# Optimization experiments

Hardware: AMD Instinct MI355X
Metric: run time of the kernel (lower is better)

The kernel has to match this reference:

```python
import jax, jax.numpy as jnp
import numpy as np

N = 100000
E = 1000000
F_NODE = 64
F_EDGE = 32
H = 128
C_NODE = 12
C_EDGE = 4


def _glorot(key, shape):
    fan_in, fan_out = shape[0], shape[1]
    s = (6.0 / (fan_in + fan_out)) ** 0.5
    return jax.random.uniform(key, shape, jnp.float32, -s, s)


def setup_inputs() -> dict:
    key = jax.random.key(0)
    ks = jax.random.split(key, 16)
    x = jax.random.normal(ks[0], (N, F_NODE), jnp.float32)
    edge_index = jax.random.randint(ks[1], (2, E), 0, N, jnp.int32)
    edge_attr = jax.random.normal(ks[2], (E, F_EDGE), jnp.float32)
    return {
        "x": x,
        "edge_index": edge_index,
        "edge_attr": edge_attr,
        "We": _glorot(ks[3], (F_NODE, H)), "be": jnp.zeros((H,), jnp.float32),
        "Wc1": _glorot(ks[4], (H, H)), "bc1": jnp.zeros((H,), jnp.float32),
        "Wc2": _glorot(ks[5], (H, H)), "bc2": jnp.zeros((H,), jnp.float32),
        "Wn1": _glorot(ks[6], (H, H // 2)), "bn1": jnp.zeros((H // 2,), jnp.float32),
        "Wn2": _glorot(ks[7], (H // 2, C_NODE)), "bn2": jnp.zeros((C_NODE,), jnp.float32),
        "Wedge1": _glorot(ks[8], (2 * H + F_EDGE, H)), "bedge1": jnp.zeros((H,), jnp.float32),
        "Wedge2": _glorot(ks[9], (H, C_EDGE)), "bedge2": jnp.zeros((C_EDGE,), jnp.float32),
    }


def _gcn_conv(x, W, b, src, tgt, n):
    # PyG GCNConv: add self-loops, symmetric deg normalization, scatter-add.
    xw = x @ W  # [N, H]
    loop = jnp.arange(n, dtype=src.dtype)
    s = jnp.concatenate([src, loop])
    t = jnp.concatenate([tgt, loop])
    deg = jax.ops.segment_sum(jnp.ones_like(t, jnp.float32), t, num_segments=n)
    dinv = jnp.where(deg > 0, jax.lax.rsqrt(jnp.maximum(deg, 1.0)), 0.0)
    norm = dinv[s] * dinv[t]  # [E+N]
    msg = xw[s] * norm[:, None]
    return jax.ops.segment_sum(msg, t, num_segments=n) + b


def reference(x, edge_index, edge_attr, We, be, Wc1, bc1, Wc2, bc2,
              Wn1, bn1, Wn2, bn2, Wedge1, bedge1, Wedge2, bedge2):
    n = x.shape[0]
    row, col = edge_index[0], edge_index[1]
    h = jax.nn.relu(x @ We + be)          # node_embed Linear+ReLU
    h = jax.nn.relu(h)                     # extra F.relu in forward
    h = jax.nn.relu(_gcn_conv(h, Wc1, bc1, row, col, n))
    h = jax.nn.relu(_gcn_conv(h, Wc2, bc2, row, col, n))
    node_logits = jax.nn.relu(h @ Wn1 + bn1) @ Wn2 + bn2
    e = jnp.concatenate([h[row], h[col], edge_attr], axis=-1)  # [E, 2H+Fe]
    edge_logits = jax.nn.relu(e @ Wedge1 + bedge1) @ Wedge2 + bedge2
    return (node_logits, edge_logits)
```

## Files before the change

### kernel.cpp

```cpp
#include <hip/hip_runtime.h>

#define N_NODES 100000
#define N_EDGES 1000000
#define NB_SCAN 391
#define EDGE_OUT_BASE 1200000

typedef __attribute__((ext_vector_type(8))) short short8;
typedef __attribute__((ext_vector_type(4))) unsigned short us4;
typedef __attribute__((ext_vector_type(4))) float f32x4;

__device__ __forceinline__ float bf2f(unsigned short u) {
    unsigned int x = ((unsigned int)u) << 16;
    return __builtin_bit_cast(float, x);
}
__device__ __forceinline__ float lo_bf(unsigned int u) {
    return __builtin_bit_cast(float, u << 16);
}
__device__ __forceinline__ float hi_bf(unsigned int u) {
    return __builtin_bit_cast(float, u & 0xffff0000u);
}
__device__ __forceinline__ unsigned short f2bf(float f) {
    unsigned int x = __builtin_bit_cast(unsigned int, f);
    return (unsigned short)((x + 0x7fffu + ((x >> 16) & 1u)) >> 16);
}

__global__ __launch_bounds__(256) void k_detect(const unsigned short* __restrict__ xr,
                                                int* __restrict__ flag) {
    __shared__ int s[256];
    int t = threadIdx.x;
    int cnt = 0;
    for (int i = t; i < 8192; i += 256) {
        int e = (xr[i] >> 7) & 0xFF;
        if (e >= 148) cnt++;
    }
    s[t] = cnt;
    __syncthreads();
    for (int off = 128; off > 0; off >>= 1) {
        if (t < off) s[t] += s[t + off];
        __syncthreads();
    }
    if (t == 0) *flag = (s[0] > 100) ? 1 : 0;
}

struct WPack { const void* p[14]; };
#define W_TOTAL 87888
__global__ __launch_bounds__(256) void k_convw(WPack wp, const int* __restrict__ flag,
                                               unsigned short* __restrict__ dst) {
    const int starts[15] = {0, 8192, 8320, 24704, 24832, 41216, 41344, 49536,
                            49600, 50368, 50380, 87244, 87372, 87884, 87888};
    bool f32 = (*flag != 0);
    int i = blockIdx.x * 256 + threadIdx.x;
    if (i >= W_TOTAL) return;
    int s = 0;
#pragma unroll
    for (int k = 1; k < 14; k++) s += (i >= starts[k]) ? 1 : 0;
    int j = i - starts[s];
    dst[i] = f32 ? f2bf(((const float*)wp.p[s])[j]) : ((const unsigned short*)wp.p[s])[j];
}
#define OW_We 0
#define OW_be 8192
#define OW_Wc1 8320
#define OW_bc1 24704
#define OW_Wc2 24832
#define OW_bc2 41216
#define OW_Wn1 41344
#define OW_bn1 49536
#define OW_Wn2 49600
#define OW_bn2 50368
#define OW_We1 50380
#define OW_be1 87244
#define OW_We2 87372
#define OW_be2 87884

__global__ __launch_bounds__(256) void k_hist(const int* __restrict__ ecol, int* __restrict__ deg) {
    int e = blockIdx.x * 256 + threadIdx.x;
    if (e < N_EDGES) atomicAdd(&deg[ecol[e]], 1);
}

__global__ __launch_bounds__(256) void k_scanA(const int* __restrict__ deg, int* __restrict__ bsum) {
    __shared__ int s[256];
    int i = blockIdx.x * 256 + threadIdx.x;
    s[threadIdx.x] = (i < N_NODES) ? deg[i] : 0;
    __syncthreads();
    for (int off = 128; off > 0; off >>= 1) {
        if (threadIdx.x < off) s[threadIdx.x] += s[threadIdx.x + off];
        __syncthreads();
    }
    if (threadIdx.x == 0) bsum[blockIdx.x] = s[0];
}

__global__ __launch_bounds__(512) void k_scanB(int* __restrict__ bsum) {
    __shared__ int s[512];
    int t = threadIdx.x;
    int v = (t < NB_SCAN) ? bsum[t] : 0;
    s[t] = v;
    __syncthreads();
    for (int off = 1; off < 512; off <<= 1) {
        int x = (t >= off) ? s[t - off] : 0;
        __syncthreads();
        s[t] += x;
        __syncthreads();
    }
    if (t < NB_SCAN) bsum[t] = s[t] - v;
}

__global__ __launch_bounds__(256) void k_scanC(const int* __restrict__ deg, const int* __restrict__ bsum,
                                               int* __restrict__ row_off, int* __restrict__ cursor,
                                               float* __restrict__ dinv) {
    __shared__ int s[256];
    int i = blockIdx.x * 256 + threadIdx.x;
    int t = threadIdx.x;
    int v = (i < N_NODES) ? deg[i] : 0;
    s[t] = v;
    __syncthreads();
    for (int off = 1; off < 256; off <<= 1) {
        int x = (t >= off) ? s[t - off] : 0;
        __syncthreads();
        s[t] += x;
        __syncthreads();
    }
    int excl = s[t] - v + bsum[blockIdx.x];
    if (i < N_NODES) {
        row_off[i] = excl;
        cursor[i] = excl;
        dinv[i] = rsqrtf((float)(v + 1));
    }
    if (i == N_NODES - 1) row_off[N_NODES] = excl + v;
}

__global__ __launch_bounds__(256) void k_fill(const int* __restrict__ erow, const int* __restrict__ ecol,
                                              int* __restrict__ cursor, int* __restrict__ csr) {
    int e = blockIdx.x * 256 + threadIdx.x;
    if (e < N_EDGES) {
        int pos = atomicAdd(&cursor[ecol[e]], 1);
        csr[pos] = erow[e];
    }
}

template <int K, int O, bool RELU, bool BIAS, bool SCALE>
__global__ __launch_bounds__(256) void gemm_rows(const void* __restrict__ A, int M,
                                                 const unsigned short* __restrict__ W, int o_real,
                                                 const unsigned short* __restrict__ bias,
                                                 void* __restrict__ Out, int out_pitch,
                                                 const float* __restrict__ rowscale,
                                                 const int* aflag, const int* oflag) {
    constexpr int KP = K + 8;
    constexpr int KS = K / 32;
    constexpr int OT = O / 16;
    __shared__ short wt[O * KP];
    __shared__ float bias_s[O];
    int tid = threadIdx.x;
    for (int idx = tid; idx < K * O; idx += 256) {
        int k = idx / O, o = idx % O;
        short w = 0;
        if (o < o_real) w = (short)W[(size_t)k * o_real + o];
        wt[o * KP + k] = w;
    }
    if (BIAS) {
        for (int o = tid; o < O; o += 256) bias_s[o] = (o < o_real) ? bf2f(bias[o]) : 0.f;
    }
    __syncthreads();

    bool af32 = aflag && (*aflag != 0);
    bool of32 = oflag && (*oflag != 0);

    int wid = tid >> 6, lane = tid & 63;
    int rbase = (blockIdx.x * 4 + wid) * 32;
    if (rbase >= M) return;
    int lq = lane >> 4, lr = lane & 15;

    short8 a[2][KS];
#pragma unroll
    for (int rg = 0; rg < 2; rg++) {
        int row = rbase + rg * 16 + lr;
        if (row >= M) row = M - 1;
        if (af32) {
            const float* ap = (const float*)A + (size_t)row * K + lq * 8;
#pragma unroll
            for (int ks = 0; ks < KS; ks++) {
                f32x4 u0 = *(const f32x4*)(ap + ks * 32);
                f32x4 u1 = *(const f32x4*)(ap + ks * 32 + 4);
                short8 v;
                v[0] = (short)f2bf(u0[0]); v[1] = (short)f2bf(u0[1]);
                v[2] = (short)f2bf(u0[2]); v[3] = (short)f2bf(u0[3]);
                v[4] = (short)f2bf(u1[0]); v[5] = (short)f2bf(u1[1]);
                v[6] = (short)f2bf(u1[2]); v[7] = (short)f2bf(u1[3]);
                a[rg][ks] = v;
            }
        } else {
            const unsigned short* ap = (const unsigned short*)A + (size_t)row * K + lq * 8;
#pragma unroll
            for (int ks = 0; ks < KS; ks++) a[rg][ks] = *(const short8*)(ap + ks * 32);
        }
    }

    f32x4 acc[2][OT];
#pragma unroll
    for (int rg = 0; rg < 2; rg++)
#pragma unroll
        for (int j = 0; j < OT; j++) {
            acc[rg][j][0] = 0.f; acc[rg][j][1] = 0.f; acc[rg][j][2] = 0.f; acc[rg][j][3] = 0.f;
        }

#pragma unroll
    for (int j = 0; j < OT; j++) {
        short8 b[KS];
#pragma unroll
        for (int ks = 0; ks < KS; ks++)
            b[ks] = *(const short8*)(&wt[(lr + 16 * j) * KP + ks * 32 + lq * 8]);
#pragma unroll
        for (int rg = 0; rg < 2; rg++)
#pragma unroll
            for (int ks = 0; ks < KS; ks++)
                acc[rg][j] = __builtin_amdgcn_mfma_f32_16x16x32_bf16(a[rg][ks], b[ks], acc[rg][j], 0, 0, 0);
    }

#pragma unroll
    for (int rg = 0; rg < 2; rg++)
#pragma unroll
        for (int j = 0; j < OT; j++)
#pragma unroll
            for (int r = 0; r < 4; r++) {
                int row = rbase + rg * 16 + lq * 4 + r;
                int col = lr + 16 * j;
                if (row < M && col < o_real) {
                    float v = acc[rg][j][r];
                    if (BIAS) v += bias_s[col];
                    if (RELU) v = fmaxf(v, 0.f);
                    if (SCALE) v *= rowscale[row];
                    size_t oi = (size_t)row * out_pitch + col;
                    if (of32) ((float*)Out)[oi] = v;
                    else ((unsigned short*)Out)[oi] = f2bf(v);
                }
            }
}

__global__ __launch_bounds__(256) void gemm_pq(const unsigned short* __restrict__ A, int M,
                                               const unsigned short* __restrict__ W1,
                                               const unsigned short* __restrict__ W2,
                                               unsigned short* __restrict__ Pout,
                                               unsigned short* __restrict__ Qout) {
    __shared__ short wt[128 * 136];
    int tid = threadIdx.x;
    int wid = tid >> 6, lane = tid & 63;
    int rbase = (blockIdx.x * 4 + wid) * 32;
    int lq = lane >> 4, lr = lane & 15;

    short8 a[2][4];
#pragma unroll
    for (int rg = 0; rg < 2; rg++) {
        int row = rbase + rg * 16 + lr;
        if (row >= M) row = M - 1;
        const unsigned short* ap = A + (size_t)row * 128 + lq * 8;
#pragma unroll
        for (int ks = 0; ks < 4; ks++) a[rg][ks] = *(const short8*)(ap + ks * 32);
    }

    int pc0 = (lr >> 2) * 32 + (lr & 3);

    for (int idx = tid; idx < 128 * 128; idx += 256) {
        int k = idx >> 7, o = idx & 127;
        wt[o * 136 + k] = (short)W1[idx];
    }
    __syncthreads();
    {
        f32x4 acc[2][8];
#pragma unroll
        for (int rg = 0; rg < 2; rg++)
#pragma unroll
            for (int j = 0; j < 8; j++) {
                acc[rg][j][0] = 0.f; acc[rg][j][1] = 0.f; acc[rg][j][2] = 0.f; acc[rg][j][3] = 0.f;
            }
#pragma unroll
        for (int j = 0; j < 8; j++) {
            short8 b[4];
#pragma unroll
            for (int ks = 0; ks < 4; ks++)
                b[ks] = *(const short8*)(&wt[(lr + 16 * j) * 136 + ks * 32 + lq * 8]);
#pragma unroll
            for (int rg = 0; rg < 2; rg++)
#pragma unroll
                for (int ks = 0; ks < 4; ks++)
                    acc[rg][j] = __builtin_amdgcn_mfma_f32_16x16x32_bf16(a[rg][ks], b[ks], acc[rg][j], 0, 0, 0);
        }
#pragma unroll
        for (int rg = 0; rg < 2; rg++)
#pragma unroll
            for (int j = 0; j < 8; j++)
#pragma unroll
                for (int r = 0; r < 4; r++) {
                    int row = rbase + rg * 16 + lq * 4 + r;
                    if (row < M) Pout[(size_t)row * 128 + pc0 + j * 4] = f2bf(acc[rg][j][r]);
                }
    }
    __syncthreads();

    for (int idx = tid; idx < 128 * 128; idx += 256) {
        int k = idx >> 7, o = idx & 127;
        wt[o * 136 + k] = (short)W2[idx];
    }
    __syncthreads();
    {
        f32x4 acc[2][8];
#pragma unroll
        for (int rg = 0; rg < 2; rg++)
#pragma unroll
            for (int j = 0; j < 8; j++) {
                acc[rg][j][0] = 0.f; acc[rg][j][1] = 0.f; acc[rg][j][2] = 0.f; acc[rg][j][3] = 0.f;
            }
#pragma unroll
        for (int j = 0; j < 8; j++) {
            short8 b[4];
#pragma unroll
            for (int ks = 0; ks < 4; ks++)
                b[ks] = *(const short8*)(&wt[(lr + 16 * j) * 136 + ks * 32 + lq * 8]);
#pragma unroll
            for (int rg = 0; rg < 2; rg++)
#pragma unroll
                for (int ks = 0; ks < 4; ks++)
                    acc[rg][j] = __builtin_amdgcn_mfma_f32_16x16x32_bf16(a[rg][ks], b[ks], acc[rg][j], 0, 0, 0);
        }
#pragma unroll
        for (int rg = 0; rg < 2; rg++)
#pragma unroll
            for (int j = 0; j < 8; j++)
#pragma unroll
                for (int r = 0; r < 4; r++) {
                    int row = rbase + rg * 16 + lq * 4 + r;
                    if (row < M) Qout[(size_t)row * 128 + pc0 + j * 4] = f2bf(acc[rg][j][r]);
                }
    }
}

__global__ __launch_bounds__(256) void conv_kernel(const unsigned short* __restrict__ xw_s,
                                                   const int* __restrict__ csr_src,
                                                   const int* __restrict__ row_off,
                                                   const float* __restrict__ dinv,
                                                   const unsigned short* __restrict__ bias,
                                                   unsigned short* __restrict__ out) {
    int wid = threadIdx.x >> 6, lane = threadIdx.x & 63;
    int base = (blockIdx.x * 4 + wid) * 2;
    int t0 = base, t1 = base + 1;
    int beg0 = row_off[t0], end0 = row_off[t0 + 1];
    int beg1 = row_off[t1], end1 = row_off[t1 + 1];
    float dt0 = dinv[t0], dt1 = dinv[t1];
    unsigned int v0 = *(const unsigned int*)(xw_s + (size_t)t0 * 128 + lane * 2);
    unsigned int v1 = *(const unsigned int*)(xw_s + (size_t)t1 * 128 + lane * 2);
    unsigned int bv = *(const unsigned int*)(bias + lane * 2);
    float a00 = lo_bf(v0), a01 = hi_bf(v0);
    float a10 = lo_bf(v1), a11 = hi_bf(v1);
    int i0 = beg0, i1 = beg1;
    while (i0 + 4 <= end0 && i1 + 4 <= end1) {
        int s00 = csr_src[i0], s01 = csr_src[i0 + 1], s02 = csr_src[i0 + 2], s03 = csr_src[i0 + 3];
        int s10 = csr_src[i1], s11 = csr_src[i1 + 1], s12 = csr_src[i1 + 2], s13 = csr_src[i1 + 3];
        unsigned int u00 = *(const unsigned int*)(xw_s + (size_t)s00 * 128 + lane * 2);
        unsigned int u01 = *(const unsigned int*)(xw_s + (size_t)s01 * 128 + lane * 2);
        unsigned int u02 = *(const unsigned int*)(xw_s + (size_t)s02 * 128 + lane * 2);
        unsigned int u03 = *(const unsigned int*)(xw_s + (size_t)s03 * 128 + lane * 2);
        unsigned int u10 = *(const unsigned int*)(xw_s + (size_t)s10 * 128 + lane * 2);
        unsigned int u11 = *(const unsigned int*)(xw_s + (size_t)s11 * 128 + lane * 2);
        unsigned int u12 = *(const unsigned int*)(xw_s + (size_t)s12 * 128 + lane * 2);
        unsigned int u13 = *(const unsigned int*)(xw_s + (size_t)s13 * 128 + lane * 2);
        a00 += lo_bf(u00) + lo_bf(u01) + lo_bf(u02) + lo_bf(u03);
        a01 += hi_bf(u00) + hi_bf(u01) + hi_bf(u02) + hi_bf(u03);
        a10 += lo_bf(u10) + lo_bf(u11) + lo_bf(u12) + lo_bf(u13);
        a11 += hi_bf(u10) + hi_bf(u11) + hi_bf(u12) + hi_bf(u13);
        i0 += 4; i1 += 4;
    }
    for (; i0 + 4 <= end0; i0 += 4) {
        int s0 = csr_src[i0], s1 = csr_src[i0 + 1], s2 = csr_src[i0 + 2], s3 = csr_src[i0 + 3];
        unsigned int u0 = *(const unsigned int*)(xw_s + (size_t)s0 * 128 + lane * 2);
        unsigned int u1 = *(const unsigned int*)(xw_s + (size_t)s1 * 128 + lane * 2);
        unsigned int u2 = *(const unsigned int*)(xw_s + (size_t)s2 * 128 + lane * 2);
        unsigned int u3 = *(const unsigned int*)(xw_s + (size_t)s3 * 128 + lane * 2);
        a00 += lo_bf(u0) + lo_bf(u1) + lo_bf(u2) + lo_bf(u3);
        a01 += hi_bf(u0) + hi_bf(u1) + hi_bf(u2) + hi_bf(u3);
    }
    for (; i1 + 4 <= end1; i1 += 4) {
        int s0 = csr_src[i1], s1 = csr_src[i1 + 1], s2 = csr_src[i1 + 2], s3 = csr_src[i1 + 3];
        unsigned int u0 = *(const unsigned int*)(xw_s + (size_t)s0 * 128 + lane * 2);
        unsigned int u1 = *(const unsigned int*)(xw_s + (size_t)s1 * 128 + lane * 2);
        unsigned int u2 = *(const unsigned int*)(xw_s + (size_t)s2 * 128 + lane * 2);
        unsigned int u3 = *(const unsigned int*)(xw_s + (size_t)s3 * 128 + lane * 2);
        a10 += lo_bf(u0) + lo_bf(u1) + lo_bf(u2) + lo_bf(u3);
        a11 += hi_bf(u0) + hi_bf(u1) + hi_bf(u2) + hi_bf(u3);
    }
    for (; i0 < end0; i0++) {
        int s = csr_src[i0];
        unsigned int u = *(const unsigned int*)(xw_s + (size_t)s * 128 + lane * 2);
        a00 += lo_bf(u); a01 += hi_bf(u);
    }
    for (; i1 < end1; i1++) {
        int s = csr_src[i1];
        unsigned int u = *(const unsigned int*)(xw_s + (size_t)s * 128 + lane * 2);
        a10 += lo_bf(u); a11 += hi_bf(u);
    }
    a00 = fmaxf(fmaf(a00, dt0, lo_bf(bv)), 0.f);
    a01 = fmaxf(fmaf(a01, dt0, hi_bf(bv)), 0.f);
    a10 = fmaxf(fmaf(a10, dt1, lo_bf(bv)), 0.f);
    a11 = fmaxf(fmaf(a11, dt1, hi_bf(bv)), 0.f);
    unsigned int o0 = (unsigned int)f2bf(a00) | ((unsigned int)f2bf(a01) << 16);
    unsigned int o1 = (unsigned int)f2bf(a10) | ((unsigned int)f2bf(a11) << 16);
    *(unsigned int*)(out + (size_t)t0 * 128 + lane * 2) = o0;
    *(unsigned int*)(out + (size_t)t1 * 128 + lane * 2) = o1;
}

__global__ __launch_bounds__(256) void edge_head(const void* __restrict__ ea,
                                                 const int* __restrict__ erow, const int* __restrict__ ecol,
                                                 const unsigned short* __restrict__ P,
                                                 const unsigned short* __restrict__ Q,
                                                 const unsigned short* __restrict__ wbuf,
                                                 void* __restrict__ out, const int* dtflag) {
    __shared__ short wct[128 * 40];
    __shared__ float w2s[128 * 4];
    __shared__ float b1s[128];
    int tid = threadIdx.x;
    const unsigned short* Wc3 = wbuf + OW_We1 + 256 * 128;
    for (int idx = tid; idx < 32 * 128; idx += 256) {
        int k = idx >> 7, o = idx & 127;
        wct[o * 40 + k] = (short)Wc3[idx];
    }
    for (int idx = tid; idx < 512; idx += 256) {
        int p = idx >> 2, o = idx & 3;
        int ch = 16 * ((p & 31) >> 2) + 4 * (p >> 5) + (p & 3);
        w2s[idx] = bf2f(wbuf[OW_We2 + ch * 4 + o]);
    }
    if (tid < 128) {
        int p = tid;
        int ch = 16 * ((p & 31) >> 2) + 4 * (p >> 5) + (p & 3);
        b1s[p] = bf2f(wbuf[OW_be1 + ch]);
    }
    __syncthreads();

    bool f32io = (*dtflag != 0);
    int wid = tid >> 6, lane = tid & 63;
    int lq = lane >> 4, lr = lane & 15;
    int tbase = (blockIdx.x * 4 + wid) * 2;
    int e0a = tbase * 16, e0b = e0a + 16;

    int gea = e0a + lr, geb = e0b + lr;
    bool va = gea < N_EDGES, vb = geb < N_EDGES;
    int geca = va ? gea : (N_EDGES - 1);
    int gecb = vb ? geb : (N_EDGES - 1);

    int rna = erow[geca], cna = ecol[geca];
    int rnb = erow[gecb], cnb = ecol[gecb];

    auto load_efrag = [&](int ge) -> short8 {
        short8 v;
        if (f32io) {
            const float* eap = (const float*)ea + (size_t)ge * 32 + lq * 8;
            f32x4 u0 = *(const f32x4*)eap;
            f32x4 u1 = *(const f32x4*)(eap + 4);
            v[0] = (short)f2bf(u0[0]); v[1] = (short)f2bf(u0[1]);
            v[2] = (short)f2bf(u0[2]); v[3] = (short)f2bf(u0[3]);
            v[4] = (short)f2bf(u1[0]); v[5] = (short)f2bf(u1[1]);
            v[6] = (short)f2bf(u1[2]); v[7] = (short)f2bf(u1[3]);
        } else {
            v = *(const short8*)((const unsigned short*)ea + (size_t)ge * 32 + lq * 8);
        }
        return v;
    };
    short8 efA = load_efrag(geca);
    short8 efB = load_efrag(gecb);

    f32x4 zero; zero[0] = 0.f; zero[1] = 0.f; zero[2] = 0.f; zero[3] = 0.f;
    f32x4 accA[8], accB[8];
#pragma unroll
    for (int j = 0; j < 8; j++) {
        short8 wfrag = *(const short8*)(&wct[(16 * j + lr) * 40 + lq * 8]);
        accA[j] = __builtin_amdgcn_mfma_f32_16x16x32_bf16(wfrag, efA, zero, 0, 0, 0);
        accB[j] = __builtin_amdgcn_mfma_f32_16x16x32_bf16(wfrag, efB, zero, 0, 0, 0);
    }

    const unsigned short* PpA = P + (size_t)rna * 128 + lq * 32;
    const unsigned short* QpA = Q + (size_t)cna * 128 + lq * 32;
    const unsigned short* PpB = P + (size_t)rnb * 128 + lq * 32;
    const unsigned short* QpB = Q + (size_t)cnb * 128 + lq * 32;
    f32x4 ovA, ovB;
    ovA[0] = 0.f; ovA[1] = 0.f; ovA[2] = 0.f; ovA[3] = 0.f;
    ovB[0] = 0.f; ovB[1] = 0.f; ovB[2] = 0.f; ovB[3] = 0.f;
#pragma unroll
    for (int c = 0; c < 4; c++) {
        short8 pvA = *(const short8*)(PpA + c * 8);
        short8 qvA = *(const short8*)(QpA + c * 8);
        short8 pvB = *(const short8*)(PpB + c * 8);
        short8 qvB = *(const short8*)(QpB + c * 8);
        int pbase = lq * 32 + c * 8;
#pragma unroll
        for (int jj = 0; jj < 2; jj++) {
            int j = 2 * c + jj;
#pragma unroll
            for (int r = 0; r < 4; r++) {
                int idx = jj * 4 + r;
                float b1v = b1s[pbase + idx];
                f32x4 w2v = *(const f32x4*)(&w2s[(pbase + idx) * 4]);
                float tA = accA[j][r] + bf2f((unsigned short)pvA[idx]) + bf2f((unsigned short)qvA[idx]) + b1v;
                tA = fmaxf(tA, 0.f);
                ovA[0] = fmaf(tA, w2v[0], ovA[0]);
                ovA[1] = fmaf(tA, w2v[1], ovA[1]);
                ovA[2] = fmaf(tA, w2v[2], ovA[2]);
                ovA[3] = fmaf(tA, w2v[3], ovA[3]);
                float tB = accB[j][r] + bf2f((unsigned short)pvB[idx]) + bf2f((unsigned short)qvB[idx]) + b1v;
                tB = fmaxf(tB, 0.f);
                ovB[0] = fmaf(tB, w2v[0], ovB[0]);
                ovB[1] = fmaf(tB, w2v[1], ovB[1]);
                ovB[2] = fmaf(tB, w2v[2], ovB[2]);
                ovB[3] = fmaf(tB, w2v[3], ovB[3]);
            }
        }
    }
#pragma unroll
    for (int c = 0; c < 4; c++) {
        ovA[c] += __shfl_xor(ovA[c], 16);
        ovA[c] += __shfl_xor(ovA[c], 32);
        ovB[c] += __shfl_xor(ovB[c], 16);
        ovB[c] += __shfl_xor(ovB[c], 32);
    }
    if (lq == 0) {
        float be2_0 = bf2f(wbuf[OW_be2 + 0]), be2_1 = bf2f(wbuf[OW_be2 + 1]);
        float be2_2 = bf2f(wbuf[OW_be2 + 2]), be2_3 = bf2f(wbuf[OW_be2 + 3]);
        if (va) {
            size_t oi = (size_t)EDGE_OUT_BASE + (size_t)gea * 4;
            if (f32io) {
                f32x4 res; res[0] = ovA[0] + be2_0; res[1] = ovA[1] + be2_1;
                res[2] = ovA[2] + be2_2; res[3] = ovA[3] + be2_3;
                *(f32x4*)((float*)out + oi) = res;
            } else {
                us4 res; res[0] = f2bf(ovA[0] + be2_0); res[1] = f2bf(ovA[1] + be2_1);
                res[2] = f2bf(ovA[2] + be2_2); res[3] = f2bf(ovA[3] + be2_3);
                *(us4*)((unsigned short*)out + oi) = res;
            }
        }
        if (vb) {
            size_t oi = (size_t)EDGE_OUT_BASE + (size_t)geb * 4;
            if (f32io) {
                f32x4 res; res[0] = ovB[0] + be2_0; res[1] = ovB[1] + be2_1;
                res[2] = ovB[2] + be2_2; res[3] = ovB[3] + be2_3;
                *(f32x4*)((float*)out + oi) = res;
            } else {
                us4 res; res[0] = f2bf(ovB[0] + be2_0); res[1] = f2bf(ovB[1] + be2_1);
                res[2] = f2bf(ovB[2] + be2_2); res[3] = f2bf(ovB[3] + be2_3);
                *(us4*)((unsigned short*)out + oi) = res;
            }
        }
    }
}

extern "C" void kernel_launch(void* const* d_in, const int* in_sizes, int n_in,
                              void* d_out, int out_size, void* d_ws, size_t ws_size,
                              hipStream_t stream) {
    const void* x = d_in[0];
    const int* ei = (const int*)d_in[1];
    const void* ea = d_in[2];
    const int* erow = ei;
    const int* ecol = ei + N_EDGES;

    char* ws = (char*)d_ws;
    size_t off = 0;
    auto alloc = [&](size_t bytes) -> void* {
        void* p = ws + off;
        off += (bytes + 255) & ~(size_t)255;
        return p;
    };
    unsigned short* Abuf = (unsigned short*)alloc((size_t)N_NODES * 128 * 2);
    unsigned short* Bbuf = (unsigned short*)alloc((size_t)N_NODES * 128 * 2);
    int* deg = (int*)alloc((size_t)N_NODES * 4);
    int* row_off = (int*)alloc((size_t)(N_NODES + 1) * 4);
    int* cursor = (int*)alloc((size_t)N_NODES * 4);
    int* csr = (int*)alloc((size_t)N_EDGES * 4);
    int* bsum = (int*)alloc(512 * 4);
    float* dinv = (float*)alloc((size_t)N_NODES * 4);
    unsigned short* wbuf = (unsigned short*)alloc((size_t)W_TOTAL * 2);
    int* dtflag = (int*)alloc(256);

    k_detect<<<1, 256, 0, stream>>>((const unsigned short*)x, dtflag);

    WPack wp;
    for (int i = 0; i < 14; i++) wp.p[i] = d_in[3 + i];
    k_convw<<<(W_TOTAL + 255) / 256, 256, 0, stream>>>(wp, dtflag, wbuf);

    (void)hipMemsetAsync(deg, 0, (size_t)N_NODES * 4, stream);
    k_hist<<<(N_EDGES + 255) / 256, 256, 0, stream>>>(ecol, deg);
    k_scanA<<<NB_SCAN, 256, 0, stream>>>(deg, bsum);
    k_scanB<<<1, 512, 0, stream>>>(bsum);
    k_scanC<<<NB_SCAN, 256, 0, stream>>>(deg, bsum, row_off, cursor, dinv);
    k_fill<<<(N_EDGES + 255) / 256, 256, 0, stream>>>(erow, ecol, cursor, csr);

    int gB = (N_NODES + 127) / 128;
    gemm_rows<64, 128, true, true, false><<<gB, 256, 0, stream>>>(x, N_NODES, wbuf + OW_We, 128, wbuf + OW_be, Abuf, 128, nullptr, dtflag, nullptr);
    gemm_rows<128, 128, false, false, true><<<gB, 256, 0, stream>>>(Abuf, N_NODES, wbuf + OW_Wc1, 128, nullptr, Bbuf, 128, dinv, nullptr, nullptr);
    conv_kernel<<<N_NODES / 8, 256, 0, stream>>>(Bbuf, csr, row_off, dinv, wbuf + OW_bc1, Abuf);
    gemm_rows<128, 128, false, false, true><<<gB, 256, 0, stream>>>(Abuf, N_NODES, wbuf + OW_Wc2, 128, nullptr, Bbuf, 128, dinv, nullptr, nullptr);
    conv_kernel<<<N_NODES / 8, 256, 0, stream>>>(Bbuf, csr, row_off, dinv, wbuf + OW_bc2, Abuf);
    gemm_rows<128, 64, true, true, false><<<gB, 256, 0, stream>>>(Abuf, N_NODES, wbuf + OW_Wn1, 64, wbuf + OW_bn1, Bbuf, 64, nullptr, nullptr, nullptr);
    gemm_rows<64, 16, false, true, false><<<gB, 256, 0, stream>>>(Bbuf, N_NODES, wbuf + OW_Wn2, 12, wbuf + OW_bn2, d_out, 12, nullptr, nullptr, dtflag);
    gemm_pq<<<gB, 256, 0, stream>>>(Abuf, N_NODES, wbuf + OW_We1, wbuf + OW_We1 + 128 * 128, Bbuf, Abuf);
    edge_head<<<(N_EDGES + 127) / 128, 256, 0, stream>>>(ea, erow, ecol, Bbuf, Abuf, wbuf, d_out, dtflag);
}
```

Before: 559.5 us.

## Fuse node-head MLP into one kernel and chunk edge-head MFMA epilogue

```diff
diff --git a/kernel.cpp b/kernel.cpp
--- a/kernel.cpp
+++ b/kernel.cpp
@@ -233,6 +233,114 @@
                     else ((unsigned short*)Out)[oi] = f2bf(v);
                 }
             }
+}
+
+__global__ __launch_bounds__(256) void node_head(const unsigned short* __restrict__ A, int M,
+                                                 const unsigned short* __restrict__ wbuf,
+                                                 void* __restrict__ Out, const int* oflag) {
+    __shared__ short wt1[64 * 136];
+    __shared__ short zb[128 * 72];
+    __shared__ short wt2[16 * 72];
+    __shared__ float b1[64];
+    __shared__ float b2[16];
+    int tid = threadIdx.x;
+    const unsigned short* Wn1 = wbuf + OW_Wn1;
+    const unsigned short* Wn2 = wbuf + OW_Wn2;
+    for (int idx = tid; idx < 64 * 128; idx += 256) {
+        int k = idx >> 6, o = idx & 63;
+        wt1[o * 136 + k] = (short)Wn1[idx];
+    }
+    for (int idx = tid; idx < 16 * 64; idx += 256) {
+        int o = idx & 15, k = idx >> 4;
+        wt2[o * 72 + k] = (o < 12) ? (short)Wn2[k * 12 + o] : 0;
+    }
+    if (tid < 64) b1[tid] = bf2f(wbuf[OW_bn1 + tid]);
+    if (tid < 16) b2[tid] = (tid < 12) ? bf2f(wbuf[OW_bn2 + tid]) : 0.f;
+    __syncthreads();
+
+    bool of32 = oflag && (*oflag != 0);
+    int wid = tid >> 6, lane = tid & 63;
+    int lq = lane >> 4, lr = lane & 15;
+    int rbase = blockIdx.x * 128 + wid * 32;
+
+    short8 a[2][4];
+#pragma unroll
+    for (int rg = 0; rg < 2; rg++) {
+        int row = rbase + rg * 16 + lr;
+        if (row >= M) row = M - 1;
+        const unsigned short* ap = A + (size_t)row * 128 + lq * 8;
+#pragma unroll
+        for (int ks = 0; ks < 4; ks++) a[rg][ks] = *(const short8*)(ap + ks * 32);
+    }
+
+    {
+        f32x4 acc[2][4];
+#pragma unroll
+        for (int rg = 0; rg < 2; rg++)
+#pragma unroll
+            for (int j = 0; j < 4; j++) {
+                acc[rg][j][0] = 0.f; acc[rg][j][1] = 0.f; acc[rg][j][2] = 0.f; acc[rg][j][3] = 0.f;
+            }
+#pragma unroll
+        for (int j = 0; j < 4; j++) {
+            short8 b[4];
+#pragma unroll
+            for (int ks = 0; ks < 4; ks++)
+                b[ks] = *(const short8*)(&wt1[(lr + 16 * j) * 136 + ks * 32 + lq * 8]);
+#pragma unroll
+            for (int rg = 0; rg < 2; rg++)
+#pragma unroll
+                for (int ks = 0; ks < 4; ks++)
+                    acc[rg][j] = __builtin_amdgcn_mfma_f32_16x16x32_bf16(a[rg][ks], b[ks], acc[rg][j], 0, 0, 0);
+        }
+#pragma unroll
+        for (int rg = 0; rg < 2; rg++)
+#pragma unroll
+            for (int j = 0; j < 4; j++)
+#pragma unroll
+                for (int r = 0; r < 4; r++) {
+                    int rl = wid * 32 + rg * 16 + lq * 4 + r;
+                    int col = lr + 16 * j;
+                    zb[rl * 72 + col] = (short)f2bf(fmaxf(acc[rg][j][r] + b1[col], 0.f));
+                }
+    }
+    __syncthreads();
+
+    {
+        short8 a2[2][2];
+#pragma unroll
+        for (int rg = 0; rg < 2; rg++) {
+            int rl = wid * 32 + rg * 16 + lr;
+#pragma unroll
+            for (int ks = 0; ks < 2; ks++)
+                a2[rg][ks] = *(const short8*)(&zb[rl * 72 + ks * 32 + lq * 8]);
+        }
+        short8 b[2];
+#pragma unroll
+        for (int ks = 0; ks < 2; ks++)
+            b[ks] = *(const short8*)(&wt2[lr * 72 + ks * 32 + lq * 8]);
+        f32x4 acc[2];
+#pragma unroll
+        for (int rg = 0; rg < 2; rg++) {
+            acc[rg][0] = 0.f; acc[rg][1] = 0.f; acc[rg][2] = 0.f; acc[rg][3] = 0.f;
+#pragma unroll
+            for (int ks = 0; ks < 2; ks++)
+                acc[rg] = __builtin_amdgcn_mfma_f32_16x16x32_bf16(a2[rg][ks], b[ks], acc[rg], 0, 0, 0);
+        }
+#pragma unroll
+        for (int rg = 0; rg < 2; rg++)
+#pragma unroll
+            for (int r = 0; r < 4; r++) {
+                int row = rbase + rg * 16 + lq * 4 + r;
+                int col = lr;
+                if (row < M && col < 12) {
+                    float v = acc[rg][r] + b2[col];
+                    size_t oi = (size_t)row * 12 + col;
+                    if (of32) ((float*)Out)[oi] = v;
+                    else ((unsigned short*)Out)[oi] = f2bf(v);
+                }
+            }
+    }
 }
 
 __global__ __launch_bounds__(256) void gemm_pq(const unsigned short* __restrict__ A, int M,
@@ -405,6 +513,27 @@
     *(unsigned int*)(out + (size_t)t1 * 128 + lane * 2) = o1;
 }
 
+__device__ __forceinline__ void epi_chunk(f32x4& ov, const f32x4& acc_lo, const f32x4& acc_hi,
+                                          short8 pv, short8 qv,
+                                          const float* __restrict__ b1s,
+                                          const float* __restrict__ w2s, int pb) {
+#pragma unroll
+    for (int jj = 0; jj < 2; jj++) {
+        const f32x4& ac = jj ? acc_hi : acc_lo;
+#pragma unroll
+        for (int r = 0; r < 4; r++) {
+            int idx = jj * 4 + r;
+            float t = ac[r] + bf2f((unsigned short)pv[idx]) + bf2f((unsigned short)qv[idx]) + b1s[pb + idx];
+            t = fmaxf(t, 0.f);
+            f32x4 w2v = *(const f32x4*)(&w2s[(pb + idx) * 4]);
+            ov[0] = fmaf(t, w2v[0], ov[0]);
+            ov[1] = fmaf(t, w2v[1], ov[1]);
+            ov[2] = fmaf(t, w2v[2], ov[2]);
+            ov[3] = fmaf(t, w2v[3], ov[3]);
+        }
+    }
+}
+
 __global__ __launch_bounds__(256) void edge_head(const void* __restrict__ ea,
                                                  const int* __restrict__ erow, const int* __restrict__ ecol,
                                                  const unsigned short* __restrict__ P,
@@ -464,52 +593,67 @@
     short8 efA = load_efrag(geca);
     short8 efB = load_efrag(gecb);
 
-    f32x4 zero; zero[0] = 0.f; zero[1] = 0.f; zero[2] = 0.f; zero[3] = 0.f;
-    f32x4 accA[8], accB[8];
-#pragma unroll
-    for (int j = 0; j < 8; j++) {
-        short8 wfrag = *(const short8*)(&wct[(16 * j + lr) * 40 + lq * 8]);
-        accA[j] = __builtin_amdgcn_mfma_f32_16x16x32_bf16(wfrag, efA, zero, 0, 0, 0);
-        accB[j] = __builtin_amdgcn_mfma_f32_16x16x32_bf16(wfrag, efB, zero, 0, 0, 0);
-    }
-
     const unsigned short* PpA = P + (size_t)rna * 128 + lq * 32;
     const unsigned short* QpA = Q + (size_t)cna * 128 + lq * 32;
     const unsigned short* PpB = P + (size_t)rnb * 128 + lq * 32;
     const unsigned short* QpB = Q + (size_t)cnb * 128 + lq * 32;
-    f32x4 ovA, ovB;
-    ovA[0] = 0.f; ovA[1] = 0.f; ovA[2] = 0.f; ovA[3] = 0.f;
-    ovB[0] = 0.f; ovB[1] = 0.f; ovB[2] = 0.f; ovB[3] = 0.f;
-#pragma unroll
-    for (int c = 0; c < 4; c++) {
-        short8 pvA = *(const short8*)(PpA + c * 8);
-        short8 qvA = *(const short8*)(QpA + c * 8);
-        short8 pvB = *(const short8*)(PpB + c * 8);
-        short8 qvB = *(const short8*)(QpB + c * 8);
-        int pbase = lq * 32 + c * 8;
-#pragma unroll
-        for (int jj = 0; jj < 2; jj++) {
-            int j = 2 * c + jj;
-#pragma unroll
-            for (int r = 0; r < 4; r++) {
-                int idx = jj * 4 + r;
-                float b1v = b1s[pbase + idx];
-                f32x4 w2v = *(const f32x4*)(&w2s[(pbase + idx) * 4]);
-                float tA = accA[j][r] + bf2f((unsigned short)pvA[idx]) + bf2f((unsigned short)qvA[idx]) + b1v;
-                tA = fmaxf(tA, 0.f);
-                ovA[0] = fmaf(tA, w2v[0], ovA[0]);
-                ovA[1] = fmaf(tA, w2v[1], ovA[1]);
-                ovA[2] = fmaf(tA, w2v[2], ovA[2]);
-                ovA[3] = fmaf(tA, w2v[3], ovA[3]);
-                float tB = accB[j][r] + bf2f((unsigned short)pvB[idx]) + bf2f((unsigned short)qvB[idx]) + b1v;
-                tB = fmaxf(tB, 0.f);
-                ovB[0] = fmaf(tB, w2v[0], ovB[0]);
-                ovB[1] = fmaf(tB, w2v[1], ovB[1]);
-                ovB[2] = fmaf(tB, w2v[2], ovB[2]);
-                ovB[3] = fmaf(tB, w2v[3], ovB[3]);
-            }
-        }
-    }
+
+    f32x4 zero; zero[0] = 0.f; zero[1] = 0.f; zero[2] = 0.f; zero[3] = 0.f;
+    f32x4 ovA = zero, ovB = zero;
+
+    {
+        short8 pA0 = *(const short8*)(PpA + 0);
+        short8 pA1 = *(const short8*)(PpA + 8);
+        short8 qA0 = *(const short8*)(QpA + 0);
+        short8 qA1 = *(const short8*)(QpA + 8);
+        short8 pB0 = *(const short8*)(PpB + 0);
+        short8 pB1 = *(const short8*)(PpB + 8);
+        short8 qB0 = *(const short8*)(QpB + 0);
+        short8 qB1 = *(const short8*)(QpB + 8);
+        short8 wf0 = *(const short8*)(&wct[(0 * 16 + lr) * 40 + lq * 8]);
+        short8 wf1 = *(const short8*)(&wct[(1 * 16 + lr) * 40 + lq * 8]);
+        short8 wf2 = *(const short8*)(&wct[(2 * 16 + lr) * 40 + lq * 8]);
+        short8 wf3 = *(const short8*)(&wct[(3 * 16 + lr) * 40 + lq * 8]);
+        f32x4 aA0 = __builtin_amdgcn_mfma_f32_16x16x32_bf16(wf0, efA, zero, 0, 0, 0);
+        f32x4 aA1 = __builtin_amdgcn_mfma_f32_16x16x32_bf16(wf1, efA, zero, 0, 0, 0);
+        f32x4 aA2 = __builtin_amdgcn_mfma_f32_16x16x32_bf16(wf2, efA, zero, 0, 0, 0);
+        f32x4 aA3 = __builtin_amdgcn_mfma_f32_16x16x32_bf16(wf3, efA, zero, 0, 0, 0);
+        f32x4 aB0 = __builtin_amdgcn_mfma_f32_16x16x32_bf16(wf0, efB, zero, 0, 0, 0);
+        f32x4 aB1 = __builtin_amdgcn_mfma_f32_16x16x32_bf16(wf1, efB, zero, 0, 0, 0);
+        f32x4 aB2 = __builtin_amdgcn_mfma_f32_16x16x32_bf16(wf2, efB, zero, 0, 0, 0);
+        f32x4 aB3 = __builtin_amdgcn_mfma_f32_16x16x32_bf16(wf3, efB, zero, 0, 0, 0);
+        epi_chunk(ovA, aA0, aA1, pA0, qA0, b1s, w2s, lq * 32 + 0);
+        epi_chunk(ovA, aA2, aA3, pA1, qA1, b1s, w2s, lq * 32 + 8);
+        epi_chunk(ovB, aB0, aB1, pB0, qB0, b1s, w2s, lq * 32 + 0);
+        epi_chunk(ovB, aB2, aB3, pB1, qB1, b1s, w2s, lq * 32 + 8);
+    }
+    {
+        short8 pA0 = *(const short8*)(PpA + 16);
+        short8 pA1 = *(const short8*)(PpA + 24);
+        short8 qA0 = *(const short8*)(QpA + 16);
+        short8 qA1 = *(const short8*)(QpA + 24);
+        short8 pB0 = *(const short8*)(PpB + 16);
+        short8 pB1 = *(const short8*)(PpB + 24);
+        short8 qB0 = *(const short8*)(QpB + 16);
+        short8 qB1 = *(const short8*)(QpB + 24);
+        short8 wf0 = *(const short8*)(&wct[(4 * 16 + lr) * 40 + lq * 8]);
+        short8 wf1 = *(const short8*)(&wct[(5 * 16 + lr) * 40 + lq * 8]);
+        short8 wf2 = *(const short8*)(&wct[(6 * 16 + lr) * 40 + lq * 8]);
+        short8 wf3 = *(const short8*)(&wct[(7 * 16 + lr) * 40 + lq * 8]);
+        f32x4 aA0 = __builtin_amdgcn_mfma_f32_16x16x32_bf16(wf0, efA, zero, 0, 0, 0);
+        f32x4 aA1 = __builtin_amdgcn_mfma_f32_16x16x32_bf16(wf1, efA, zero, 0, 0, 0);
+        f32x4 aA2 = __builtin_amdgcn_mfma_f32_16x16x32_bf16(wf2, efA, zero, 0, 0, 0);
+        f32x4 aA3 = __builtin_amdgcn_mfma_f32_16x16x32_bf16(wf3, efA, zero, 0, 0, 0);
+        f32x4 aB0 = __builtin_amdgcn_mfma_f32_16x16x32_bf16(wf0, efB, zero, 0, 0, 0);
+        f32x4 aB1 = __builtin_amdgcn_mfma_f32_16x16x32_bf16(wf1, efB, zero, 0, 0, 0);
+        f32x4 aB2 = __builtin_amdgcn_mfma_f32_16x16x32_bf16(wf2, efB, zero, 0, 0, 0);
+        f32x4 aB3 = __builtin_amdgcn_mfma_f32_16x16x32_bf16(wf3, efB, zero, 0, 0, 0);
+        epi_chunk(ovA, aA0, aA1, pA0, qA0, b1s, w2s, lq * 32 + 16);
+        epi_chunk(ovA, aA2, aA3, pA1, qA1, b1s, w2s, lq * 32 + 24);
+        epi_chunk(ovB, aB0, aB1, pB0, qB0, b1s, w2s, lq * 32 + 16);
+        epi_chunk(ovB, aB2, aB3, pB1, qB1, b1s, w2s, lq * 32 + 24);
+    }
+
 #pragma unroll
     for (int c = 0; c < 4; c++) {
         ovA[c] += __shfl_xor(ovA[c], 16);
@@ -593,8 +737,7 @@
     conv_kernel<<<N_NODES / 8, 256, 0, stream>>>(Bbuf, csr, row_off, dinv, wbuf + OW_bc1, Abuf);
     gemm_rows<128, 128, false, false, true><<<gB, 256, 0, stream>>>(Abuf, N_NODES, wbuf + OW_Wc2, 128, nullptr, Bbuf, 128, dinv, nullptr, nullptr);
     conv_kernel<<<N_NODES / 8, 256, 0, stream>>>(Bbuf, csr, row_off, dinv, wbuf + OW_bc2, Abuf);
-    gemm_rows<128, 64, true, true, false><<<gB, 256, 0, stream>>>(Abuf, N_NODES, wbuf + OW_Wn1, 64, wbuf + OW_bn1, Bbuf, 64, nullptr, nullptr, nullptr);
-    gemm_rows<64, 16, false, true, false><<<gB, 256, 0, stream>>>(Bbuf, N_NODES, wbuf + OW_Wn2, 12, wbuf + OW_bn2, d_out, 12, nullptr, nullptr, dtflag);
+    node_head<<<gB, 256, 0, stream>>>(Abuf, N_NODES, wbuf, d_out, dtflag);
     gemm_pq<<<gB, 256, 0, stream>>>(Abuf, N_NODES, wbuf + OW_We1, wbuf + OW_We1 + 128 * 128, Bbuf, Abuf);
     edge_head<<<(N_EDGES + 127) / 128, 256, 0, stream>>>(ea, erow, ecol, Bbuf, Abuf, wbuf, d_out, dtflag);
 }
```

Measured after the change: 538.8 us. 3.7% less time.
